# Performance work log

Measured on AMD Instinct MI355X. Metric: run time of the kernel, lower is better.

Reference implementation:

```python
import jax, jax.numpy as jnp
import numpy as np

IN_F = 8192
OUT_F = 8192
MAX_STATES = 100
THRESHOLD = MAX_STATES // 2  # 50


def setup_inputs() -> dict:
    key = jax.random.key(0)
    k1, k2 = jax.random.split(key, 2)
    spike_input = (jax.random.uniform(k1, (IN_F,)) < 0.2).astype(jnp.float32)
    # synapse states as in __init__: randn*5 + threshold, clamped to [1, max_states]
    synapse_states = jnp.clip(
        jax.random.normal(k2, (OUT_F, IN_F)) * 5.0 + THRESHOLD, 1.0, float(MAX_STATES)
    ).astype(jnp.float32)
    membrane_potential = jnp.zeros((OUT_F,), jnp.float32)
    adaptive_threshold = jnp.full((OUT_F,), 3.0, jnp.float32)
    eligibility_trace = jnp.zeros((OUT_F, IN_F), jnp.float32)
    refractory_period = jnp.zeros((OUT_F,), jnp.float32)
    return {
        "spike_input": spike_input,
        "synapse_states": synapse_states,
        "membrane_potential": membrane_potential,
        "adaptive_threshold": adaptive_threshold,
        "eligibility_trace": eligibility_trace,
        "refractory_period": refractory_period,
    }


def reference(spike_input, synapse_states, membrane_potential, adaptive_threshold,
              eligibility_trace, refractory_period):
    # Ternary (effectively binary 0/1) weights from synapse states
    w = (synapse_states > float(THRESHOLD)).astype(jnp.float32)  # [out, in]
    x = spike_input.reshape(-1)                                   # [in]
    current = w @ x                                               # [out]
    # LIF membrane update with refractory gating
    v_mem = membrane_potential * 0.5 + current * (1.0 - refractory_period * 0.5)
    spikes = (v_mem >= adaptive_threshold).astype(jnp.float32)    # [out]
    # Eligibility trace: decay + outer-product accumulation + clamp
    new_trace = jnp.clip(eligibility_trace * 0.8 + jnp.outer(spikes, x), 0.0, 5.0)
    # Refractory update
    new_refractory = jnp.clip(refractory_period + spikes - 0.1, 0.0, 1.0)
    # Membrane reset where spiked
    new_membrane = v_mem * (1.0 - spikes)
    return spikes, new_membrane, new_trace, new_refractory
```

## Files before the change

### kernel.cpp

```cpp
#include <hip/hip_runtime.h>


#define IN_F 8192
#define OUT_F 8192
#define BLOCK 256
#define VEC_ITERS (IN_F / 4 / BLOCK)

__global__ __launch_bounds__(BLOCK) void snn_fused_kernel(
    const float* __restrict__ x_in,
    const float* __restrict__ syn,
    const float* __restrict__ mem,
    const float* __restrict__ thr,
    const float* __restrict__ trace,
    const float* __restrict__ refr,
    float* __restrict__ out_spikes,
    float* __restrict__ out_mem,
    float* __restrict__ out_trace,
    float* __restrict__ out_refr)
{
    const int row = blockIdx.x;
    const int tid = threadIdx.x;

    __shared__ float4 sx[IN_F / 4];
    __shared__ float s_partial[BLOCK / 64];

    const float4* __restrict__ x4 = (const float4*)x_in;
    const float4* __restrict__ syn4 =
        (const float4*)(syn + (size_t)row * IN_F);

    #pragma unroll
    for (int it = 0; it < VEC_ITERS; ++it) {
        sx[it * BLOCK + tid] = x4[it * BLOCK + tid];
    }
    __syncthreads();

    float acc = 0.0f;
    #pragma unroll
    for (int it = 0; it < VEC_ITERS; ++it) {
        const int idx = it * BLOCK + tid;
        const float4 s = syn4[idx];
        const float4 xv = sx[idx];
        acc += (s.x > 50.0f) ? xv.x : 0.0f;
        acc += (s.y > 50.0f) ? xv.y : 0.0f;
        acc += (s.z > 50.0f) ? xv.z : 0.0f;
        acc += (s.w > 50.0f) ? xv.w : 0.0f;
    }
    #pragma unroll
    for (int off = 32; off > 0; off >>= 1) {
        acc += __shfl_down(acc, off, 64);
    }
    if ((tid & 63) == 0) s_partial[tid >> 6] = acc;
    __syncthreads();

    const float current =
        s_partial[0] + s_partial[1] + s_partial[2] + s_partial[3];

    const float r = refr[row];
    const float v = mem[row] * 0.5f + current * (1.0f - r * 0.5f);
    const float spike = (v >= thr[row]) ? 1.0f : 0.0f;
    if (tid == 0) {
        out_spikes[row] = spike;
        out_mem[row] = v * (1.0f - spike);
        out_refr[row] = fminf(fmaxf(r + spike - 0.1f, 0.0f), 1.0f);
    }

    const float4* __restrict__ tr4 =
        (const float4*)(trace + (size_t)row * IN_F);
    float4* __restrict__ otr4 = (float4*)(out_trace + (size_t)row * IN_F);
    #pragma unroll
    for (int it = 0; it < VEC_ITERS; ++it) {
        const int idx = it * BLOCK + tid;
        const float4 t = tr4[idx];
        const float4 xv = sx[idx];
        float4 o;
        o.x = fminf(fmaxf(t.x * 0.8f + spike * xv.x, 0.0f), 5.0f);
        o.y = fminf(fmaxf(t.y * 0.8f + spike * xv.y, 0.0f), 5.0f);
        o.z = fminf(fmaxf(t.z * 0.8f + spike * xv.z, 0.0f), 5.0f);
        o.w = fminf(fmaxf(t.w * 0.8f + spike * xv.w, 0.0f), 5.0f);
        otr4[idx] = o;
    }
}

extern "C" void kernel_launch(void* const* d_in, const int* in_sizes, int n_in,
                              void* d_out, int out_size, void* d_ws, size_t ws_size,
                              hipStream_t stream) {
    const float* x_in  = (const float*)d_in[0];
    const float* syn   = (const float*)d_in[1];
    const float* mem   = (const float*)d_in[2];
    const float* thr   = (const float*)d_in[3];
    const float* trace = (const float*)d_in[4];
    const float* refr  = (const float*)d_in[5];

    float* out = (float*)d_out;
    float* out_spikes = out;
    float* out_mem    = out + OUT_F;
    float* out_trace  = out + 2 * OUT_F;
    float* out_refr   = out + 2 * OUT_F + (size_t)OUT_F * IN_F;

    snn_fused_kernel<<<OUT_F, BLOCK, 0, stream>>>(
        x_in, syn, mem, thr, trace, refr,
        out_spikes, out_mem, out_trace, out_refr);
}
```

Measured before the change: 592.4 us.

## Split fused SNN kernel into wave-per-row matvec and separate trace kernel

Splits the single fused kernel into a matvec kernel where each wavefront handles one row with no shared memory or block barriers, and a separate trace-update kernel that reads spikes from the first kernel's output. The intent is to remove the per-row x staging in LDS and the __syncthreads stalls so each phase streams global memory with better occupancy. In exchange it adds a second kernel launch and gives up the fusion of the two phases, and x is reread from global memory or cache in both kernels.

```diff
diff --git a/kernel.cpp b/kernel.cpp
--- a/kernel.cpp
+++ b/kernel.cpp
@@ -4,42 +4,30 @@
 #define IN_F 8192
 #define OUT_F 8192
 #define BLOCK 256
-#define VEC_ITERS (IN_F / 4 / BLOCK)
 
-__global__ __launch_bounds__(BLOCK) void snn_fused_kernel(
-    const float* __restrict__ x_in,
+__global__ __launch_bounds__(BLOCK) void snn_matvec_kernel(
+    const float4* __restrict__ x4,
     const float* __restrict__ syn,
     const float* __restrict__ mem,
     const float* __restrict__ thr,
-    const float* __restrict__ trace,
     const float* __restrict__ refr,
     float* __restrict__ out_spikes,
     float* __restrict__ out_mem,
-    float* __restrict__ out_trace,
     float* __restrict__ out_refr)
 {
-    const int row = blockIdx.x;
-    const int tid = threadIdx.x;
+    const int wave = threadIdx.x >> 6;
+    const int lane = threadIdx.x & 63;
+    const int row  = (blockIdx.x << 2) + wave;
 
-    __shared__ float4 sx[IN_F / 4];
-    __shared__ float s_partial[BLOCK / 64];
-
-    const float4* __restrict__ x4 = (const float4*)x_in;
     const float4* __restrict__ syn4 =
         (const float4*)(syn + (size_t)row * IN_F);
 
-    #pragma unroll
-    for (int it = 0; it < VEC_ITERS; ++it) {
-        sx[it * BLOCK + tid] = x4[it * BLOCK + tid];
-    }
-    __syncthreads();
-
     float acc = 0.0f;
-    #pragma unroll
-    for (int it = 0; it < VEC_ITERS; ++it) {
-        const int idx = it * BLOCK + tid;
-        const float4 s = syn4[idx];
-        const float4 xv = sx[idx];
+    #pragma unroll 8
+    for (int it = 0; it < IN_F / 4 / 64; ++it) {
+        const int idx = (it << 6) + lane;
+        const float4 s  = syn4[idx];
+        const float4 xv = x4[idx];
         acc += (s.x > 50.0f) ? xv.x : 0.0f;
         acc += (s.y > 50.0f) ? xv.y : 0.0f;
         acc += (s.z > 50.0f) ? xv.z : 0.0f;
@@ -49,35 +37,37 @@
     for (int off = 32; off > 0; off >>= 1) {
         acc += __shfl_down(acc, off, 64);
     }
-    if ((tid & 63) == 0) s_partial[tid >> 6] = acc;
-    __syncthreads();
+    if (lane == 0) {
+        const float r = refr[row];
+        const float v = mem[row] * 0.5f + acc * (1.0f - r * 0.5f);
+        const float spike = (v >= thr[row]) ? 1.0f : 0.0f;
+        out_spikes[row] = spike;
+        out_mem[row]    = v * (1.0f - spike);
+        out_refr[row]   = fminf(fmaxf(r + spike - 0.1f, 0.0f), 1.0f);
+    }
+}
 
-    const float current =
-        s_partial[0] + s_partial[1] + s_partial[2] + s_partial[3];
+__global__ __launch_bounds__(BLOCK) void snn_trace_kernel(
+    const float4* __restrict__ x4,
+    const float4* __restrict__ tr4,
+    const float* __restrict__ spikes,
+    float4* __restrict__ otr4)
+{
+    const int row = blockIdx.x;
+    const float spike = spikes[row];
+    const size_t base = (size_t)row * (IN_F / 4);
 
-    const float r = refr[row];
-    const float v = mem[row] * 0.5f + current * (1.0f - r * 0.5f);
-    const float spike = (v >= thr[row]) ? 1.0f : 0.0f;
-    if (tid == 0) {
-        out_spikes[row] = spike;
-        out_mem[row] = v * (1.0f - spike);
-        out_refr[row] = fminf(fmaxf(r + spike - 0.1f, 0.0f), 1.0f);
-    }
-
-    const float4* __restrict__ tr4 =
-        (const float4*)(trace + (size_t)row * IN_F);
-    float4* __restrict__ otr4 = (float4*)(out_trace + (size_t)row * IN_F);
     #pragma unroll
-    for (int it = 0; it < VEC_ITERS; ++it) {
-        const int idx = it * BLOCK + tid;
-        const float4 t = tr4[idx];
-        const float4 xv = sx[idx];
+    for (int it = 0; it < IN_F / 4 / BLOCK; ++it) {
+        const int idx = it * BLOCK + threadIdx.x;
+        const float4 t  = tr4[base + idx];
+        const float4 xv = x4[idx];
         float4 o;
         o.x = fminf(fmaxf(t.x * 0.8f + spike * xv.x, 0.0f), 5.0f);
         o.y = fminf(fmaxf(t.y * 0.8f + spike * xv.y, 0.0f), 5.0f);
         o.z = fminf(fmaxf(t.z * 0.8f + spike * xv.z, 0.0f), 5.0f);
         o.w = fminf(fmaxf(t.w * 0.8f + spike * xv.w, 0.0f), 5.0f);
-        otr4[idx] = o;
+        otr4[base + idx] = o;
     }
 }
 
@@ -97,7 +87,11 @@
     float* out_trace  = out + 2 * OUT_F;
     float* out_refr   = out + 2 * OUT_F + (size_t)OUT_F * IN_F;
 
-    snn_fused_kernel<<<OUT_F, BLOCK, 0, stream>>>(
-        x_in, syn, mem, thr, trace, refr,
-        out_spikes, out_mem, out_trace, out_refr);
+    snn_matvec_kernel<<<OUT_F / 4, BLOCK, 0, stream>>>(
+        (const float4*)x_in, syn, mem, thr, refr,
+        out_spikes, out_mem, out_refr);
+
+    snn_trace_kernel<<<OUT_F, BLOCK, 0, stream>>>(
+        (const float4*)x_in, (const float4*)trace, out_spikes,
+        (float4*)out_trace);
 }
```

Measured after the change: 587.2 us. Within noise of the previous version (-0.9%).
